# Kernel tuning notes

Measured on AMD Instinct MI355X. Metric: run time of the kernel, lower is better.

The kernel has to match this reference:

```python
import jax, jax.numpy as jnp
import numpy as np

MARGIN = 0.5
EPS = 1e-5
NEG_TOPK = 10  # cfg.XBM.NEG_TOPK; memory path (B != M) uses top-k negatives


def setup_inputs() -> dict:
    key = jax.random.key(0)
    k1, k2, k3, k4 = jax.random.split(key, 4)
    B, M, D, C = 256, 65536, 512, 1000
    inputs_col = jax.random.normal(k1, (B, D), dtype=jnp.float32)
    inputs_row = jax.random.normal(k2, (M, D), dtype=jnp.float32)
    targets_col = jax.random.randint(k3, (B,), 0, C)
    target_row = jax.random.randint(k4, (M,), 0, C)
    return {
        "inputs_col": inputs_col,
        "targets_col": targets_col,
        "inputs_row": inputs_row,
        "target_row": target_row,
    }


def reference(inputs_col, targets_col, inputs_row, target_row):
    # sim_mat: [B, M] dense similarity
    sim = jnp.matmul(inputs_col, inputs_row.T)
    same = targets_col[:, None] == target_row[None, :]  # [B, M]

    # positive pairs: same label and sim < 1 - eps; loss = sum(1 - sim)
    pos_mask = same & (sim < 1.0 - EPS)
    pos_loss = jnp.sum(jnp.where(pos_mask, 1.0 - sim, 0.0), axis=1)  # [B]

    # negative pairs (B != M memory path): top-k largest similarities among
    # different-label entries; loss = sum of those top-k values.
    neg_vals = jnp.where(same, -jnp.inf, sim)  # [B, M]
    topk_vals, _ = jax.lax.top_k(neg_vals, NEG_TOPK)  # [B, k]
    neg_loss = jnp.sum(jnp.where(jnp.isfinite(topk_vals), topk_vals, 0.0), axis=1)

    # loss = sum_i (pos_loss_i + neg_loss_i) / n
    return jnp.mean(pos_loss + neg_loss)
```

## Files before the change

### kernel.cpp

```cpp
#include <hip/hip_runtime.h>
#include <math.h>
#include <float.h>

typedef __attribute__((ext_vector_type(4))) float f32x4;
typedef __attribute__((ext_vector_type(8))) __bf16 bf16x8;
typedef __attribute__((ext_vector_type(4))) __bf16 bf16x4;

#define NEG_TOPK 10
#define BROW 256
#define MT 64
#define BK 64
#define SIMSTR 72
#define ABYTES 32768
#define BUF 40960

__device__ __forceinline__ void topk_ins(float (&top)[NEG_TOPK], float v) {
    #pragma unroll
    for (int q = NEG_TOPK - 1; q >= 1; --q)
        top[q] = fmaxf(fminf(v, top[q - 1]), top[q]);
    top[0] = fmaxf(top[0], v);
}

__device__ __forceinline__ bf16x4 cvt4(float4 v) {
    bf16x4 r;
    r[0] = (__bf16)v.x; r[1] = (__bf16)v.y;
    r[2] = (__bf16)v.z; r[3] = (__bf16)v.w;
    return r;
}

__global__ __launch_bounds__(256) void cl_pass0(
    const float* __restrict__ A, char* __restrict__ A_swz, int D)
{
    const int idx = blockIdx.x * 256 + threadIdx.x;
    const int r    = idx >> 7;
    const int rem  = idx & 127;
    const int step = rem >> 4;
    const int g    = rem & 15;
    float4 v = ((const float4*)A)[r * (D >> 2) + rem];
    bf16x4 b = cvt4(v);
    const int off = step * ABYTES + r * 128 + ((g * 8) ^ ((r & 7) << 4));
    *(unsigned long long*)(A_swz + off) = *(unsigned long long*)&b;
}

__global__ __launch_bounds__(512, 2) void cl_pass1(
    const char* __restrict__ A_swz,
    const float* __restrict__ Bm,
    const int* __restrict__ tcol,
    const int* __restrict__ trow,
    float* __restrict__ part_topk,
    float* __restrict__ pos_part,
    int D)
{
    __shared__ char smem[2 * BUF];

    const int mb = blockIdx.x;
    const int j0 = mb * MT;
    const int t  = threadIdx.x;
    const int wave = t >> 6, lane = t & 63;
    const int wr = wave >> 1, wc = wave & 1;
    const int lrow = lane & 15, lk = lane >> 4;

    const float4* B4 = (const float4*)Bm;
    const int ldq = D >> 2;
    const int NSTEP = D / BK;

    const int rb = t >> 4;
    const int k4 = t & 15;

    f32x4 acc[4][2];
    #pragma unroll
    for (int m = 0; m < 4; ++m)
        #pragma unroll
        for (int n = 0; n < 2; ++n)
            acc[m][n] = (f32x4){0.f, 0.f, 0.f, 0.f};

    float4 brA[2], brB[2];

    const char* gA = A_swz + wave * 4096 + lane * 16;
    char* lA0 = smem + wave * 4096;
    char* lA1 = smem + BUF + wave * 4096;

    const int swz = (lrow & 7) << 4;

#define GLDS_A(STEP, LP)                                                       \
    {                                                                          \
        const char* gp_ = gA + (STEP) * ABYTES;                                \
        _Pragma("unroll")                                                      \
        for (int q = 0; q < 4; ++q)                                            \
            __builtin_amdgcn_global_load_lds(                                  \
                (const __attribute__((address_space(1))) void*)(gp_ + q*1024), \
                (__attribute__((address_space(3))) void*)((LP) + q*1024),      \
                16, 0, 0);                                                     \
        __builtin_amdgcn_sched_barrier(0);                                     \
    }

#define LOAD_B(STEP, SET)                                                      \
    {                                                                          \
        const int kq_ = (STEP) * (BK / 4);                                     \
        _Pragma("unroll")                                                      \
        for (int s = 0; s < 2; ++s)                                            \
            SET[s] = B4[(size_t)(j0 + rb + 32 * s) * ldq + kq_ + k4];          \
        __builtin_amdgcn_sched_barrier(0);                                     \
    }

#define STAGE_B(BUFP, SET)                                                     \
    {                                                                          \
        char* Bb_ = (BUFP) + ABYTES;                                           \
        _Pragma("unroll")                                                      \
        for (int s = 0; s < 2; ++s) {                                          \
            int r_ = rb + 32 * s;                                              \
            *(bf16x4*)(Bb_ + r_ * 128 + ((k4 * 8) ^ ((r_ & 7) << 4))) =        \
                cvt4(SET[s]);                                                  \
        }                                                                      \
    }

#define COMPUTE(BUFP)                                                          \
    {                                                                          \
        const char* Ab_ = (BUFP);                                              \
        const char* Bb_ = Ab_ + ABYTES;                                        \
        _Pragma("unroll")                                                      \
        for (int ks = 0; ks < 2; ++ks) {                                       \
            bf16x8 af[4], bfr[2];                                              \
            const int kb_ = ks * 64 + lk * 16;                                 \
            _Pragma("unroll")                                                  \
            for (int m = 0; m < 4; ++m) {                                      \
                int row_ = wr * 64 + m * 16 + lrow;                            \
                af[m] = *(const bf16x8*)(Ab_ + row_ * 128 + (kb_ ^ swz));      \
            }                                                                  \
            _Pragma("unroll")                                                  \
            for (int n = 0; n < 2; ++n) {                                      \
                int row_ = wc * 32 + n * 16 + lrow;                            \
                bfr[n] = *(const bf16x8*)(Bb_ + row_ * 128 + (kb_ ^ swz));     \
            }                                                                  \
            _Pragma("unroll")                                                  \
            for (int m = 0; m < 4; ++m)                                        \
                _Pragma("unroll")                                              \
                for (int n = 0; n < 2; ++n)                                    \
                    acc[m][n] = __builtin_amdgcn_mfma_f32_16x16x32_bf16(       \
                        af[m], bfr[n], acc[m][n], 0, 0, 0);                    \
        }                                                                      \
    }

#define DRAIN_BARRIER(CNT)                                                     \
    asm volatile("s_waitcnt vmcnt(" #CNT ") lgkmcnt(0)" ::: "memory");         \
    __builtin_amdgcn_s_barrier();                                              \
    __builtin_amdgcn_sched_barrier(0);

    GLDS_A(0, lA0);
    LOAD_B(0, brA);
    LOAD_B(1, brB);
    STAGE_B(smem, brA);

    for (int step = 0; step < NSTEP; step += 2) {
        if (step < NSTEP - 1) { DRAIN_BARRIER(2) } else { DRAIN_BARRIER(0) }
        if (step + 1 < NSTEP) GLDS_A(step + 1, lA1);
        if (step + 2 < NSTEP) LOAD_B(step + 2, brA);
        COMPUTE(smem);
        if (step + 1 < NSTEP) STAGE_B(smem + BUF, brB);

        if (step + 1 < NSTEP) {
            if (step + 1 < NSTEP - 1) { DRAIN_BARRIER(2) } else { DRAIN_BARRIER(0) }
            if (step + 2 < NSTEP) GLDS_A(step + 2, lA0);
            if (step + 3 < NSTEP) LOAD_B(step + 3, brB);
            COMPUTE(smem + BUF);
            if (step + 2 < NSTEP) STAGE_B(smem, brA);
        }
    }
    DRAIN_BARRIER(0)

    unsigned short* simsb = (unsigned short*)smem;
    #pragma unroll
    for (int m = 0; m < 4; ++m)
        #pragma unroll
        for (int n = 0; n < 2; ++n)
            #pragma unroll
            for (int r = 0; r < 4; ++r) {
                int row = wr * 64 + m * 16 + lk * 4 + r;
                int col = wc * 32 + n * 16 + lrow;
                __bf16 b = (__bf16)acc[m][n][r];
                simsb[row * SIMSTR + col] = *(unsigned short*)&b;
            }
    __syncthreads();

    {
        const int row = t >> 1, half = t & 1;
        const int myc = tcol[row];
        const int4* lab4 = (const int4*)(trow + j0 + half * 32);
        float top[NEG_TOPK];
        #pragma unroll
        for (int q = 0; q < NEG_TOPK; ++q) top[q] = -INFINITY;
        float pos = 0.f;
        #pragma unroll
        for (int j = 0; j < 4; ++j) {
            bf16x8 v8 = *(const bf16x8*)(&simsb[row * SIMSTR + half * 32 + j * 8]);
            int4 l1 = lab4[2 * j], l2 = lab4[2 * j + 1];
            int lab[8] = {l1.x, l1.y, l1.z, l1.w, l2.x, l2.y, l2.z, l2.w};
            #pragma unroll
            for (int e = 0; e < 8; ++e) {
                float s = (float)v8[e];
                bool same = (lab[e] == myc);
                pos += (same && s < 0.99999f) ? (1.f - s) : 0.f;
                topk_ins(top, same ? -INFINITY : s);
            }
        }
        float* mtop = (float*)(smem + BUF);
        float* mpos = (float*)(smem + BUF + 20480);
        #pragma unroll
        for (int q = 0; q < NEG_TOPK; ++q) mtop[t * NEG_TOPK + q] = top[q];
        mpos[t] = pos;
        __syncthreads();
        if (half == 0) {
            const float* ot = &mtop[(t + 1) * NEG_TOPK];
            #pragma unroll
            for (int q = 0; q < NEG_TOPK; ++q) topk_ins(top, ot[q]);
            float post = pos + mpos[t + 1];
            float* dst = part_topk + ((size_t)row * gridDim.x + mb) * NEG_TOPK;
            #pragma unroll
            for (int q = 0; q < NEG_TOPK; ++q) dst[q] = top[q];
            pos_part[(size_t)row * gridDim.x + mb] = post;
        }
    }
}

__global__ __launch_bounds__(256) void cl_pass2(
    const float* __restrict__ part_topk,
    const float* __restrict__ pos_part,
    float* __restrict__ row_tot,
    int nch)
{
    const int i = blockIdx.x;
    const int t = threadIdx.x;
    __shared__ float stop[256][NEG_TOPK];
    __shared__ float stop2[32][NEG_TOPK];
    __shared__ float red[256];

    const int n = nch * NEG_TOPK;
    const float* src = part_topk + (size_t)i * n;
    float top[NEG_TOPK];
    #pragma unroll
    for (int q = 0; q < NEG_TOPK; ++q) top[q] = -INFINITY;
    for (int idx = t; idx < n; idx += 256) topk_ins(top, src[idx]);
    #pragma unroll
    for (int q = 0; q < NEG_TOPK; ++q) stop[t][q] = top[q];

    float pos = 0.0f;
    const float* psrc = pos_part + (size_t)i * nch;
    for (int idx = t; idx < nch; idx += 256) pos += psrc[idx];
    red[t] = pos;
    __syncthreads();

    for (int s2 = 128; s2 >= 1; s2 >>= 1) {
        if (t < s2) red[t] += red[t + s2];
        __syncthreads();
    }

    if (t < 32) {
        float m[NEG_TOPK];
        #pragma unroll
        for (int q = 0; q < NEG_TOPK; ++q) m[q] = -INFINITY;
        for (int l = 0; l < 8; ++l)
            #pragma unroll
            for (int q = 0; q < NEG_TOPK; ++q) topk_ins(m, stop[t * 8 + l][q]);
        #pragma unroll
        for (int q = 0; q < NEG_TOPK; ++q) stop2[t][q] = m[q];
    }
    __syncthreads();

    if (t == 0) {
        float m[NEG_TOPK];
        #pragma unroll
        for (int q = 0; q < NEG_TOPK; ++q) m[q] = -INFINITY;
        for (int l = 0; l < 32; ++l)
            #pragma unroll
            for (int q = 0; q < NEG_TOPK; ++q) topk_ins(m, stop2[l][q]);
        float neg = 0.0f;
        #pragma unroll
        for (int q = 0; q < NEG_TOPK; ++q)
            if (isfinite(m[q])) neg += m[q];
        row_tot[i] = neg + red[0];
    }
}

__global__ __launch_bounds__(256) void cl_pass3(
    const float* __restrict__ row_tot, float* __restrict__ out, int Bn)
{
    __shared__ float red[256];
    const int t = threadIdx.x;
    float v = 0.0f;
    for (int idx = t; idx < Bn; idx += 256) v += row_tot[idx];
    red[t] = v;
    __syncthreads();
    for (int s2 = 128; s2 >= 1; s2 >>= 1) {
        if (t < s2) red[t] += red[t + s2];
        __syncthreads();
    }
    if (t == 0) out[0] = red[0] / (float)Bn;
}

extern "C" void kernel_launch(void* const* d_in, const int* in_sizes, int n_in,
                              void* d_out, int out_size, void* d_ws, size_t ws_size,
                              hipStream_t stream)
{
    const float* A    = (const float*)d_in[0];
    const int*   tcol = (const int*)d_in[1];
    const float* Bm   = (const float*)d_in[2];
    const int*   trow = (const int*)d_in[3];
    float* out = (float*)d_out;

    const int Bn = in_sizes[1];
    const int M  = in_sizes[3];
    const int D  = in_sizes[0] / Bn;
    const int numMB = M / MT;
    const int nch = numMB;

    char* A_swz = (char*)d_ws;
    float* part_topk = (float*)(A_swz + 8 * ABYTES);
    float* pos_part  = part_topk + (size_t)Bn * nch * NEG_TOPK;
    float* row_tot   = pos_part + (size_t)Bn * nch;

    cl_pass0<<<128, 256, 0, stream>>>(A, A_swz, D);
    cl_pass1<<<numMB, 512, 0, stream>>>(A_swz, Bm, tcol, trow,
                                        part_topk, pos_part, D);
    cl_pass2<<<Bn, 256, 0, stream>>>(part_topk, pos_part, row_tot, nch);
    cl_pass3<<<1, 256, 0, stream>>>(row_tot, out, Bn);
}
```

Measured before the change: 254.7 us.

## Widen M tile to 128 with reworked double-buffered pipeline and per-half partials

Doubles the number of memory-row columns each block handles (MT 64 to 128), so each wave computes a 64x64 output tile with 4x4 MFMAs. The A operand, staged once in LDS, is now reused across twice as many B rows and the block count is halved. The K loop is restructured: fragment reads, async A loads, B staging and B prefetch are interleaved between two MFMA groups, with s_setprio raised during MFMA. The in-block merge of the two half-row top-k lists is dropped, so each half writes its own partial and pass2 reduces twice as many chunks. In exchange, register use rises with 16 accumulators and pass2 has more partials to merge.

Result: no change. 257.4 us (+1.1%).

```diff
diff --git a/kernel.cpp b/kernel.cpp
--- a/kernel.cpp
+++ b/kernel.cpp
@@ -7,12 +7,12 @@
 typedef __attribute__((ext_vector_type(4))) __bf16 bf16x4;
 
 #define NEG_TOPK 10
-#define BROW 256
-#define MT 64
+#define MT 128
 #define BK 64
-#define SIMSTR 72
+#define SIMSTR 136
 #define ABYTES 32768
-#define BUF 40960
+#define BBYTES 16384
+#define TBUF (ABYTES + BBYTES)
 
 __device__ __forceinline__ void topk_ins(float (&top)[NEG_TOPK], float v) {
     #pragma unroll
@@ -51,7 +51,7 @@
     float* __restrict__ pos_part,
     int D)
 {
-    __shared__ char smem[2 * BUF];
+    __shared__ char smem[2 * TBUF];
 
     const int mb = blockIdx.x;
     const int j0 = mb * MT;
@@ -64,119 +64,121 @@
     const int ldq = D >> 2;
     const int NSTEP = D / BK;
 
-    const int rb = t >> 4;
-    const int k4 = t & 15;
-
-    f32x4 acc[4][2];
+    const int rB = t >> 2;
+    const int cB = t & 3;
+
+    f32x4 acc[4][4];
     #pragma unroll
     for (int m = 0; m < 4; ++m)
         #pragma unroll
-        for (int n = 0; n < 2; ++n)
+        for (int n = 0; n < 4; ++n)
             acc[m][n] = (f32x4){0.f, 0.f, 0.f, 0.f};
 
-    float4 brA[2], brB[2];
+    float4 b0[4], b1[4];
 
     const char* gA = A_swz + wave * 4096 + lane * 16;
-    char* lA0 = smem + wave * 4096;
-    char* lA1 = smem + BUF + wave * 4096;
+    char* buf0 = smem;
+    char* buf1 = smem + TBUF;
 
     const int swz = (lrow & 7) << 4;
-
-#define GLDS_A(STEP, LP)                                                       \
+    const int bswzr = (rB & 7) << 4;
+
+#define LOAD_B(STEP, SET)                                                      \
+    {                                                                          \
+        const int kq_ = (STEP) * (BK / 4);                                     \
+        _Pragma("unroll")                                                      \
+        for (int s = 0; s < 4; ++s)                                            \
+            SET[s] = B4[(size_t)(j0 + rB) * ldq + kq_ + cB + 4 * s];           \
+    }
+
+#define STAGE_B(BUFP, SET)                                                     \
+    {                                                                          \
+        char* Bb_ = (BUFP) + ABYTES;                                           \
+        _Pragma("unroll")                                                      \
+        for (int s = 0; s < 4; ++s)                                            \
+            *(bf16x4*)(Bb_ + rB * 128 + (((cB + 4 * s) * 8) ^ bswzr)) =        \
+                cvt4(SET[s]);                                                  \
+    }
+
+#define GLDS_A(STEP, BUFP)                                                     \
     {                                                                          \
         const char* gp_ = gA + (STEP) * ABYTES;                                \
+        char* lp_ = (BUFP) + wave * 4096;                                      \
         _Pragma("unroll")                                                      \
         for (int q = 0; q < 4; ++q)                                            \
             __builtin_amdgcn_global_load_lds(                                  \
                 (const __attribute__((address_space(1))) void*)(gp_ + q*1024), \
-                (__attribute__((address_space(3))) void*)((LP) + q*1024),      \
+                (__attribute__((address_space(3))) void*)(lp_ + q*1024),       \
                 16, 0, 0);                                                     \
+    }
+
+#define DS_FRAGS(BUFP, KB, AF, BF)                                             \
+    _Pragma("unroll")                                                          \
+    for (int m = 0; m < 4; ++m)                                                \
+        AF[m] = *(const bf16x8*)((BUFP) + (wr * 64 + m * 16 + lrow) * 128      \
+                                 + (((KB) + lk * 16) ^ swz));                  \
+    _Pragma("unroll")                                                          \
+    for (int n = 0; n < 4; ++n)                                                \
+        BF[n] = *(const bf16x8*)((BUFP) + ABYTES                               \
+                                 + (wc * 64 + n * 16 + lrow) * 128             \
+                                 + (((KB) + lk * 16) ^ swz));
+
+#define MFMA16(AF, BF)                                                         \
+    __builtin_amdgcn_s_setprio(1);                                             \
+    _Pragma("unroll")                                                          \
+    for (int m = 0; m < 4; ++m)                                                \
+        _Pragma("unroll")                                                      \
+        for (int n = 0; n < 4; ++n)                                            \
+            acc[m][n] = __builtin_amdgcn_mfma_f32_16x16x32_bf16(               \
+                AF[m], BF[n], acc[m][n], 0, 0, 0);                             \
+    __builtin_amdgcn_s_setprio(0);
+
+#define TILE(T, CURB, NXTB, WSET, LSET)                                        \
+    {                                             \
+        bf16x8 af0[4], bf0[4];                                                 \
+        DS_FRAGS(CURB, 0, af0, bf0);                                           \
+        if ((T) + 1 < NSTEP) GLDS_A((T) + 1, NXTB);                            \
+        MFMA16(af0, bf0);                                                      \
+        __builtin_amdgcn_s_barrier();                                          \
+    }                                                                          \
+    {                        \
+        bf16x8 af1[4], bf1[4];                                                 \
+        DS_FRAGS(CURB, 64, af1, bf1);                                          \
+        if ((T) + 1 < NSTEP) STAGE_B(NXTB, WSET);                              \
+        if ((T) + 2 < NSTEP) LOAD_B((T) + 2, LSET);                            \
+        MFMA16(af1, bf1);                                                      \
         __builtin_amdgcn_sched_barrier(0);                                     \
-    }
-
-#define LOAD_B(STEP, SET)                                                      \
-    {                                                                          \
-        const int kq_ = (STEP) * (BK / 4);                                     \
-        _Pragma("unroll")                                                      \
-        for (int s = 0; s < 2; ++s)                                            \
-            SET[s] = B4[(size_t)(j0 + rb + 32 * s) * ldq + kq_ + k4];          \
+        if ((T) + 2 < NSTEP) {                                                 \
+            asm volatile("s_waitcnt vmcnt(4) lgkmcnt(0)" ::: "memory");        \
+        } else {                                                               \
+            asm volatile("s_waitcnt vmcnt(0) lgkmcnt(0)" ::: "memory");        \
+        }                                                                      \
+        __builtin_amdgcn_s_barrier();                                          \
         __builtin_amdgcn_sched_barrier(0);                                     \
     }
 
-#define STAGE_B(BUFP, SET)                                                     \
-    {                                                                          \
-        char* Bb_ = (BUFP) + ABYTES;                                           \
-        _Pragma("unroll")                                                      \
-        for (int s = 0; s < 2; ++s) {                                          \
-            int r_ = rb + 32 * s;                                              \
-            *(bf16x4*)(Bb_ + r_ * 128 + ((k4 * 8) ^ ((r_ & 7) << 4))) =        \
-                cvt4(SET[s]);                                                  \
-        }                                                                      \
-    }
-
-#define COMPUTE(BUFP)                                                          \
-    {                                                                          \
-        const char* Ab_ = (BUFP);                                              \
-        const char* Bb_ = Ab_ + ABYTES;                                        \
-        _Pragma("unroll")                                                      \
-        for (int ks = 0; ks < 2; ++ks) {                                       \
-            bf16x8 af[4], bfr[2];                                              \
-            const int kb_ = ks * 64 + lk * 16;                                 \
-            _Pragma("unroll")                                                  \
-            for (int m = 0; m < 4; ++m) {                                      \
-                int row_ = wr * 64 + m * 16 + lrow;                            \
-                af[m] = *(const bf16x8*)(Ab_ + row_ * 128 + (kb_ ^ swz));      \
-            }                                                                  \
-            _Pragma("unroll")                                                  \
-            for (int n = 0; n < 2; ++n) {                                      \
-                int row_ = wc * 32 + n * 16 + lrow;                            \
-                bfr[n] = *(const bf16x8*)(Bb_ + row_ * 128 + (kb_ ^ swz));     \
-            }                                                                  \
-            _Pragma("unroll")                                                  \
-            for (int m = 0; m < 4; ++m)                                        \
-                _Pragma("unroll")                                              \
-                for (int n = 0; n < 2; ++n)                                    \
-                    acc[m][n] = __builtin_amdgcn_mfma_f32_16x16x32_bf16(       \
-                        af[m], bfr[n], acc[m][n], 0, 0, 0);                    \
-        }                                                                      \
-    }
-
-#define DRAIN_BARRIER(CNT)                                                     \
-    asm volatile("s_waitcnt vmcnt(" #CNT ") lgkmcnt(0)" ::: "memory");         \
-    __builtin_amdgcn_s_barrier();                                              \
+    GLDS_A(0, buf0);
+    LOAD_B(0, b0);
+    LOAD_B(1, b1);
+    STAGE_B(buf0, b0);
+    asm volatile("s_waitcnt vmcnt(0) lgkmcnt(0)" ::: "memory");
+    __builtin_amdgcn_s_barrier();
     __builtin_amdgcn_sched_barrier(0);
 
-    GLDS_A(0, lA0);
-    LOAD_B(0, brA);
-    LOAD_B(1, brB);
-    STAGE_B(smem, brA);
-
-    for (int step = 0; step < NSTEP; step += 2) {
-        if (step < NSTEP - 1) { DRAIN_BARRIER(2) } else { DRAIN_BARRIER(0) }
-        if (step + 1 < NSTEP) GLDS_A(step + 1, lA1);
-        if (step + 2 < NSTEP) LOAD_B(step + 2, brA);
-        COMPUTE(smem);
-        if (step + 1 < NSTEP) STAGE_B(smem + BUF, brB);
-
-        if (step + 1 < NSTEP) {
-            if (step + 1 < NSTEP - 1) { DRAIN_BARRIER(2) } else { DRAIN_BARRIER(0) }
-            if (step + 2 < NSTEP) GLDS_A(step + 2, lA0);
-            if (step + 3 < NSTEP) LOAD_B(step + 3, brB);
-            COMPUTE(smem + BUF);
-            if (step + 2 < NSTEP) STAGE_B(smem, brA);
-        }
-    }
-    DRAIN_BARRIER(0)
+    for (int tt = 0; tt < NSTEP; tt += 2) {
+        TILE(tt,     buf0, buf1, b1, b0)
+        TILE(tt + 1, buf1, buf0, b0, b1)
+    }
 
     unsigned short* simsb = (unsigned short*)smem;
     #pragma unroll
     for (int m = 0; m < 4; ++m)
         #pragma unroll
-        for (int n = 0; n < 2; ++n)
+        for (int n = 0; n < 4; ++n)
             #pragma unroll
             for (int r = 0; r < 4; ++r) {
                 int row = wr * 64 + m * 16 + lk * 4 + r;
-                int col = wc * 32 + n * 16 + lrow;
+                int col = wc * 64 + n * 16 + lrow;
                 __bf16 b = (__bf16)acc[m][n][r];
                 simsb[row * SIMSTR + col] = *(unsigned short*)&b;
             }
@@ -185,14 +187,14 @@
     {
         const int row = t >> 1, half = t & 1;
         const int myc = tcol[row];
-        const int4* lab4 = (const int4*)(trow + j0 + half * 32);
+        const int4* lab4 = (const int4*)(trow + j0 + half * 64);
         float top[NEG_TOPK];
         #pragma unroll
         for (int q = 0; q < NEG_TOPK; ++q) top[q] = -INFINITY;
         float pos = 0.f;
         #pragma unroll
-        for (int j = 0; j < 4; ++j) {
-            bf16x8 v8 = *(const bf16x8*)(&simsb[row * SIMSTR + half * 32 + j * 8]);
+        for (int j = 0; j < 8; ++j) {
+            bf16x8 v8 = *(const bf16x8*)(&simsb[row * SIMSTR + half * 64 + j * 8]);
             int4 l1 = lab4[2 * j], l2 = lab4[2 * j + 1];
             int lab[8] = {l1.x, l1.y, l1.z, l1.w, l2.x, l2.y, l2.z, l2.w};
             #pragma unroll
@@ -203,22 +205,12 @@
                 topk_ins(top, same ? -INFINITY : s);
             }
         }
-        float* mtop = (float*)(smem + BUF);
-        float* mpos = (float*)(smem + BUF + 20480);
-        #pragma unroll
-        for (int q = 0; q < NEG_TOPK; ++q) mtop[t * NEG_TOPK + q] = top[q];
-        mpos[t] = pos;
-        __syncthreads();
-        if (half == 0) {
-            const float* ot = &mtop[(t + 1) * NEG_TOPK];
-            #pragma unroll
-            for (int q = 0; q < NEG_TOPK; ++q) topk_ins(top, ot[q]);
-            float post = pos + mpos[t + 1];
-            float* dst = part_topk + ((size_t)row * gridDim.x + mb) * NEG_TOPK;
-            #pragma unroll
-            for (int q = 0; q < NEG_TOPK; ++q) dst[q] = top[q];
-            pos_part[(size_t)row * gridDim.x + mb] = post;
-        }
+        const int nch = 2 * gridDim.x;
+        const int ch = mb * 2 + half;
+        float* dst = part_topk + ((size_t)row * nch + ch) * NEG_TOPK;
+        #pragma unroll
+        for (int q = 0; q < NEG_TOPK; ++q) dst[q] = top[q];
+        pos_part[(size_t)row * nch + ch] = pos;
     }
 }
 
@@ -311,7 +303,7 @@
     const int M  = in_sizes[3];
     const int D  = in_sizes[0] / Bn;
     const int numMB = M / MT;
-    const int nch = numMB;
+    const int nch = numMB * 2;
 
     char* A_swz = (char*)d_ws;
     float* part_topk = (float*)(A_swz + 8 * ABYTES);
```
